# Performance work log

Measured on AMD Instinct MI355X. Metric: run time of the kernel, lower is better.

Reference implementation:

```python
import jax, jax.numpy as jnp
import numpy as np

N = 50000          # site nodes
L = 32             # max URL token length
E = 64             # embed_size
H = 128            # hidden_size
E_SIM = 800000     # edges per relation in blocks
E_SUB = 200000     # 'sim' edges classified at the end
NEG = 0.01         # LeakyReLU negative slope

def leaky(x):
    return jnp.where(x >= 0, x, NEG * x)

def lstm_final(x, mask, Wih, Whh, b, reverse):
    # x: [N, L, E], mask: [N, L] bool. Returns packed-sequence final hidden [N, E].
    if reverse:
        x = x[:, ::-1, :]
        mask = mask[:, ::-1]
    h0 = jnp.zeros((x.shape[0], Whh.shape[1]), x.dtype)
    def step(carry, inp):
        h, c = carry
        xt, mt = inp
        g = xt @ Wih.T + h @ Whh.T + b
        i, f, gg, o = jnp.split(g, 4, axis=-1)  # PyTorch gate order i,f,g,o
        cn = jax.nn.sigmoid(f) * c + jax.nn.sigmoid(i) * jnp.tanh(gg)
        hn = jax.nn.sigmoid(o) * jnp.tanh(cn)
        m = mt[:, None]
        return (jnp.where(m, hn, h), jnp.where(m, cn, c)), None
    (h, _), _ = jax.lax.scan(step, (h0, h0), (x.transpose(1, 0, 2), mask.T))
    return h

def graph_conv(h, src, dst, W, b):
    # DGL GraphConv, norm='both': D_dst^{-1/2} A D_src^{-1/2} h W + b  (degrees clamped to >=1)
    n = h.shape[0]
    ones = jnp.ones(src.shape[0], h.dtype)
    out_deg = jnp.clip(jax.ops.segment_sum(ones, src, num_segments=n), 1.0)
    in_deg = jnp.clip(jax.ops.segment_sum(ones, dst, num_segments=n), 1.0)
    feat = h * jax.lax.rsqrt(out_deg)[:, None]
    if W.shape[0] > W.shape[1]:
        feat = feat @ W  # project before gather/scatter when in_dim > out_dim (as DGL does)
        rst = jax.ops.segment_sum(feat[src], dst, num_segments=n)
    else:
        rst = jax.ops.segment_sum(feat[src], dst, num_segments=n) @ W
    return rst * jax.lax.rsqrt(in_deg)[:, None] + b

def setup_inputs():
    key = jax.random.key(0)
    ks = iter(jax.random.split(key, 64))
    def nrm(shape, scale=0.05):
        return jax.random.normal(next(ks), shape, dtype=jnp.float32) * scale
    inp = {}
    inp["inputs_s"] = jax.random.randint(next(ks), (N, L), 0, 128)
    lengths = jax.random.randint(next(ks), (N,), 1, L + 1)
    inp["inputs_sm"] = (jnp.arange(L)[None, :] < lengths[:, None]).astype(jnp.int32)
    inp["inputs_c"] = jax.random.randint(next(ks), (N, 1), 0, 101)
    inp["inputs_co"] = jax.random.randint(next(ks), (N, 1), 0, 92)
    inp["inputs_sl"] = jax.random.randint(next(ks), (N, 1), 0, 6)
    for name, m in [("sim_src", E_SIM), ("sim_dst", E_SIM), ("user_src", E_SIM),
                    ("user_dst", E_SIM), ("esub_src", E_SUB), ("esub_dst", E_SUB)]:
        inp[name] = jax.random.randint(next(ks), (m,), 0, N)
    inp["emb_url"] = nrm((128, E)); inp["emb_cat"] = nrm((101, E))
    inp["emb_country"] = nrm((92, E)); inp["emb_sl"] = nrm((6, E))
    for d in ("f", "b"):
        inp["Wih_" + d] = nrm((4 * E, E)); inp["Whh_" + d] = nrm((4 * E, E))
        inp["b_" + d] = nrm((4 * E,))  # b_ih + b_hh folded into one bias
    inp["fc_W"] = nrm((E, 2 * E)); inp["fc_b"] = nrm((E,))
    for i, din in enumerate([4 * E, H]):
        for rel in ("sim", "user"):
            inp["gcn%d_%s_W" % (i, rel)] = nrm((din, H))
            inp["gcn%d_%s_b" % (i, rel)] = nrm((H,))
    inp["cls_W1"] = nrm((H, 2 * H)); inp["cls_b1"] = nrm((H,))
    inp["bn_g"] = jnp.ones((H,), jnp.float32); inp["bn_b"] = jnp.zeros((H,), jnp.float32)
    inp["cls_W2"] = nrm((2, H)); inp["cls_b2"] = nrm((2,))
    return inp

def reference(inputs_s, inputs_sm, inputs_c, inputs_co, inputs_sl,
              sim_src, sim_dst, user_src, user_dst, esub_src, esub_dst,
              emb_url, emb_cat, emb_country, emb_sl,
              Wih_f, Whh_f, b_f, Wih_b, Whh_b, b_b, fc_W, fc_b,
              gcn0_sim_W, gcn0_sim_b, gcn0_user_W, gcn0_user_b,
              gcn1_sim_W, gcn1_sim_b, gcn1_user_W, gcn1_user_b,
              cls_W1, cls_b1, bn_g, bn_b, cls_W2, cls_b2):
    mask = inputs_sm.astype(bool)
    x = emb_url[inputs_s]                                # [N, L, E]
    hf = lstm_final(x, mask, Wih_f, Whh_f, b_f, False)   # h_n[0]
    hb = lstm_final(x, mask, Wih_b, Whh_b, b_b, True)    # h_n[1]
    h_url = leaky(jnp.concatenate([hf, hb], -1) @ fc_W.T + fc_b)  # dropout = identity (eval)
    h = jnp.concatenate([h_url, emb_cat[inputs_c[:, 0]],
                         emb_country[inputs_co[:, 0]], emb_sl[inputs_sl[:, 0]]], -1)  # [N, 4E]
    layers = [(gcn0_sim_W, gcn0_sim_b, gcn0_user_W, gcn0_user_b),
              (gcn1_sim_W, gcn1_sim_b, gcn1_user_W, gcn1_user_b)]
    for Ws, bs, Wu, bu in layers:  # HeteroGraphConv aggregate='sum'
        h = leaky(graph_conv(h, sim_src, sim_dst, Ws, bs)
                  + graph_conv(h, user_src, user_dst, Wu, bu))
    feat = jnp.concatenate([h[esub_src], h[esub_dst]], -1)  # [E_SUB, 2H]
    z = feat @ cls_W1.T + cls_b1
    z = (z - z.mean(0)) * jax.lax.rsqrt(z.var(0) + 1e-5) * bn_g + bn_b  # BatchNorm1d (batch stats)
    z = jnp.maximum(z, 0.0)
    return z @ cls_W2.T + cls_b2
```

## Files before the change

kernel.cpp:

```cpp
#include <hip/hip_runtime.h>
#include <hip/hip_bf16.h>
#include <stdint.h>

#define N_NODES 50000
#define SEQ_L   32
#define NE_BIG  800000
#define NE_SUB  200000
#define DSTRIDE 64

typedef __hip_bfloat16 bf16;
typedef unsigned short u16;
typedef _Float16 f16;
typedef _Float16 v8h __attribute__((ext_vector_type(8)));
typedef float v4f __attribute__((ext_vector_type(4)));

__device__ __forceinline__ float b2f(bf16 x) { return __bfloat162float(x); }
__device__ __forceinline__ float leakyf(float v) { return v >= 0.f ? v : 0.01f * v; }
__device__ __forceinline__ u16 f2h_bits(float x) { f16 h = (f16)x; u16 b; __builtin_memcpy(&b, &h, 2); return b; }
__device__ __forceinline__ float h2f(u16 b) { f16 h; __builtin_memcpy(&h, &b, 2); return (float)h; }
__device__ __forceinline__ uint pack2h(float a, float b) { return (uint)f2h_bits(a) | ((uint)f2h_bits(b) << 16); }

__device__ __forceinline__ float ldf(const void* p, int i, int isbf) {
  return isbf ? b2f(((const bf16*)p)[i]) : ((const float*)p)[i];
}

__device__ __forceinline__ int detect_isbf(const u16* __restrict__ u) {
  __shared__ int insane;
  if (threadIdx.x == 0) insane = 0;
  __syncthreads();
  int expo = (u[threadIdx.x * 2] >> 7) & 0xFF;
  if (expo >= 147) atomicAdd(&insane, 1);
  __syncthreads();
  return insane == 0;
}

struct PrepArgs {
  const void* Whh_f; const void* Whh_b; const void* fc_W; const void* cls_W1;
  const void* g0sW; const void* g0uW; const void* g1sW; const void* g1uW;
  const void* emb_cat; const void* emb_country; const void* emb_sl;
  const void* fc_b; const void* cls_b1; const void* g0sb; const void* g0ub;
  const void* g1sb; const void* g1ub; const void* bn_g; const void* bn_b;
  const void* cls_W2; const void* cls_b2;
  const void* emb_url; const void* Wih_f; const void* b_f; const void* Wih_b; const void* b_b;
  f16* Whh_h; u16* Bfc; u16* BW1; u16* Bg0; u16* Bg1;
  u16* embc_h; u16* embco_h; u16* embs_h;
  float* fcb; float* b1; float* g0sbP; float* g0ubP; float* g1sbP; float* g1ubP;
  float* bngP; float* bnbP; float* W2P; float* b2P;
  int* cnt4; int* cnt33; int* cur33; float* bnsums; int* dflag;
  float* Xperm;
};

__global__ __launch_bounds__(256) void prep_mega_kernel(PrepArgs A) {
  const int b = blockIdx.x;
  const int t = threadIdx.x;
  const int isbf = detect_isbf((const u16*)A.emb_url);
  auto cpy = [&](const void* s, float* d, int n, int boff) {
    int i = (b - boff) * 256 + t;
    if (i < n) d[i] = ldf(s, i, isbf);
  };
  auto cvh = [&](const void* s, u16* d, int n, int boff) {
    int i = (b - boff) * 256 + t;
    if (i < n) d[i] = f2h_bits(ldf(s, i, isbf));
  };
  auto trh = [&](const void* s, u16* d, int R, int C, int KOFF, int boff) {
    int i = (b - boff) * 256 + t;
    if (i < R * C) { int r = i / C, c = i % C; d[c * 256 + KOFF + r] = f2h_bits(ldf(s, i, isbf)); }
  };
  if      (b <   64) cvh(A.Whh_f, (u16*)A.Whh_h, 16384, 0);
  else if (b <  128) cvh(A.Whh_b, (u16*)(A.Whh_h + 16384), 16384, 64);
  else if (b <  160) cvh(A.fc_W, A.Bfc, 8192, 128);
  else if (b <  288) cvh(A.cls_W1, A.BW1, 32768, 160);
  else if (b <  416) trh(A.g0sW, A.Bg0, 256, 128, 0, 288);
  else if (b <  544) trh(A.g0uW, A.Bg0 + 128 * 256, 256, 128, 0, 416);
  else if (b <  608) trh(A.g1sW, A.Bg1, 128, 128, 0, 544);
  else if (b <  672) trh(A.g1uW, A.Bg1, 128, 128, 128, 608);
  else if (b <  698) cvh(A.emb_cat, A.embc_h, 6464, 672);
  else if (b <  721) cvh(A.emb_country, A.embco_h, 5888, 698);
  else if (b <  723) cvh(A.emb_sl, A.embs_h, 384, 721);
  else if (b <  724) cpy(A.fc_b, A.fcb, 64, 723);
  else if (b <  725) cpy(A.cls_b1, A.b1, 128, 724);
  else if (b <  726) cpy(A.g0sb, A.g0sbP, 128, 725);
  else if (b <  727) cpy(A.g0ub, A.g0ubP, 128, 726);
  else if (b <  728) cpy(A.g1sb, A.g1sbP, 128, 727);
  else if (b <  729) cpy(A.g1ub, A.g1ubP, 128, 728);
  else if (b <  730) cpy(A.bn_g, A.bngP, 128, 729);
  else if (b <  731) cpy(A.bn_b, A.bnbP, 128, 730);
  else if (b <  732) cpy(A.cls_W2, A.W2P, 256, 731);
  else if (b <  733) cpy(A.cls_b2, A.b2P, 2, 732);
  else if (b < 1515) {
    int i = (b - 733) * 256 + t;
    if (i < 4 * N_NODES) A.cnt4[i] = 0;
  } else if (b < 1516) {
    if (t < 64) { A.cnt33[t] = 0; A.cur33[t] = 0; }
    A.bnsums[t] = 0.f;
    if (t == 0) A.dflag[0] = isbf;
  } else {
    int bb = b - 1516;
    int dir = bb >> 7;
    int v = bb & 127;
    const void* Wih = dir ? A.Wih_b : A.Wih_f;
    const void* bias = dir ? A.b_b : A.b_f;
    __shared__ float embL[64];
    if (t < 64) embL[t] = ldf(A.emb_url, v * 64 + t, isbf);
    __syncthreads();
    float acc = ldf(bias, t, isbf);
#pragma unroll 8
    for (int j = 0; j < 64; ++j) acc += embL[j] * ldf(Wih, t * 64 + j, isbf);
    int g = t >> 6, unit = t & 63;
    A.Xperm[(size_t)dir * 128 * 256 + v * 256 + unit * 4 + g] = acc;
  }
}
#define PREP_BLOCKS 1772

__global__ __launch_bounds__(256) void graph_build_kernel(
    const int* __restrict__ sm, int* __restrict__ lens, int* __restrict__ cnt33,
    const int* __restrict__ s0, const int* __restrict__ d0,
    const int* __restrict__ s1, const int* __restrict__ d1,
    int* __restrict__ cnt4, int* __restrict__ col0, int* __restrict__ col1)
{
  const int b = blockIdx.x, t = threadIdx.x;
  const int NBL = (N_NODES + 255) / 256;
  const int NBE = (NE_BIG + 255) / 256;
  if (b < NBL) {
    int i = b * 256 + t;
    if (i >= N_NODES) return;
    int len = 0;
#pragma unroll
    for (int tt = 0; tt < SEQ_L; ++tt) len += sm[i * SEQ_L + tt];
    lens[i] = len;
    atomicAdd(&cnt33[len], 1);
  } else {
    int rel = (b - NBL) / NBE;
    int e = ((b - NBL) % NBE) * 256 + t;
    if (e >= NE_BIG) return;
    const int* s = rel ? s1 : s0;
    const int* d = rel ? d1 : d0;
    int* col = rel ? col1 : col0;
    int* base = cnt4 + (size_t)rel * 2 * N_NODES;
    int sv = s[e], dv = d[e];
    atomicAdd(&base[sv], 1);
    int p = atomicAdd(&base[N_NODES + dv], 1);
    if (p < DSTRIDE) col[(size_t)dv * DSTRIDE + p] = sv;
  }
}
#define GB_BLOCKS (196 + 2 * 3125)

__global__ __launch_bounds__(256) void permfill_rsq_kernel(
    const int* __restrict__ lens, const int* __restrict__ cnt33, int* __restrict__ cur33,
    int* __restrict__ perm,
    const int* __restrict__ cnt4, float* __restrict__ rsq4)
{
  const int b = blockIdx.x, t = threadIdx.x;
  const int NBL = (N_NODES + 255) / 256;
  if (b < NBL) {
    int i = b * 256 + t;
    if (i >= N_NODES) return;
    int len = lens[i];
    int base = 0;
    for (int l = len + 1; l <= SEQ_L; ++l) base += cnt33[l];
    int p = atomicAdd(&cur33[len], 1);
    perm[base + p] = i;
  } else {
    int i = (b - NBL) * 256 + t;
    if (i >= 4 * N_NODES) return;
    int c = cnt4[i]; if (c < 1) c = 1;
    rsq4[i] = __builtin_amdgcn_rsqf((float)c);
  }
}
#define PR_BLOCKS (196 + 782)

__global__ __launch_bounds__(256, 3) void lstm_mfma_kernel(
    const int* __restrict__ perm, const int* __restrict__ lens,
    const int* __restrict__ toksg,
    const float* __restrict__ Xperm,
    const f16* __restrict__ Whh_h,
    u16* __restrict__ hcat_h,
    int nnodes)
{
  __shared__ __align__(16) f16 H[2][64 * 72];
  __shared__ int toksL[2][64];
  __shared__ int permL[64];
  __shared__ int lensL[64];
  __shared__ int smax;
  const int tid = threadIdx.x;
  const int w = tid >> 6;
  const int lane = tid & 63;
  const int quad = lane >> 4;
  const int lid = lane & 15;
  const int dir = blockIdx.y;

  if (tid < 64) {
    int gid = blockIdx.x * 64 + tid;
    int node = -1, len = 0;
    if (gid < nnodes) { node = perm[gid]; len = lens[node]; }
    permL[tid] = node; lensL[tid] = len;
  }
  if (tid == 0) smax = 0;
  for (int i = tid; i < 64 * 72; i += 256) { H[0][i] = (f16)0.f; H[1][i] = (f16)0.f; }
  __syncthreads();
  if (tid < 64 && lensL[tid] > 0) atomicMax(&smax, lensL[tid]);
  __syncthreads();
  const int tmax = smax;

  const f16* Wd = Whh_h + (size_t)dir * 256 * 64;
  v8h Bf[4][2];
#pragma unroll
  for (int g = 0; g < 4; ++g)
#pragma unroll
    for (int kf = 0; kf < 2; ++kf)
      Bf[g][kf] = *(const v8h*)(Wd + (g * 64 + w * 16 + lid) * 64 + kf * 32 + quad * 8);

  int lenv[16];
#pragma unroll
  for (int mt = 0; mt < 4; ++mt)
#pragma unroll
    for (int r = 0; r < 4; ++r) lenv[mt * 4 + r] = lensL[mt * 16 + quad * 4 + r];

  float creg[16];
  f16 hreg[16];
#pragma unroll
  for (int i = 0; i < 16; ++i) { creg[i] = 0.f; hreg[i] = (f16)0.f; }

  const float* Xp = Xperm + (size_t)dir * 128 * 256;

  if (tid < 64) {
    int len = lensL[tid];
    int tok = 0;
    if (len > 0) tok = toksg[(size_t)permL[tid] * SEQ_L + (dir ? (len - 1) : 0)];
    toksL[0][tid] = tok;
  }
  __syncthreads();

  for (int step = 0; step < tmax; ++step) {
    const int rb = step & 1, wb = rb ^ 1;
#pragma unroll
    for (int mt = 0; mt < 4; ++mt) {
      float4 xr[4];
#pragma unroll
      for (int r = 0; r < 4; ++r) {
        int nd = mt * 16 + quad * 4 + r;
        xr[r] = *(const float4*)(Xp + (size_t)toksL[rb][nd] * 256 + (w * 16 + lid) * 4);
      }
      const f16* hb = &H[rb][0];
      int arow = (mt * 16 + lid) * 72 + quad * 8;
      v8h a0 = *(const v8h*)(hb + arow);
      v8h a1 = *(const v8h*)(hb + arow + 32);
      v4f acc[4];
#pragma unroll
      for (int g = 0; g < 4; ++g) {
        v4f a = {0.f, 0.f, 0.f, 0.f};
        a = __builtin_amdgcn_mfma_f32_16x16x32_f16(a0, Bf[g][0], a, 0, 0, 0);
        a = __builtin_amdgcn_mfma_f32_16x16x32_f16(a1, Bf[g][1], a, 0, 0, 0);
        acc[g] = a;
      }
#pragma unroll
      for (int r = 0; r < 4; ++r) {
        int idx = mt * 4 + r;
        int nd = mt * 16 + quad * 4 + r;
        bool act = step < lenv[idx];
        float gi = acc[0][r] + xr[r].x;
        float gf = acc[1][r] + xr[r].y;
        float gG = acc[2][r] + xr[r].z;
        float go = acc[3][r] + xr[r].w;
        float A = __expf(-gi);
        float B = __expf(-gf);
        float C = __expf(-go);
        float D = __expf(2.f * fminf(gG, 15.f));
        float sf = __builtin_amdgcn_rcpf(1.f + B);
        float sitg = (D - 1.f) * __builtin_amdgcn_rcpf((1.f + A) * (D + 1.f));
        float cn = sf * creg[idx] + sitg;
        float E = __expf(2.f * fminf(cn, 15.f));
        float hn = (E - 1.f) * __builtin_amdgcn_rcpf((1.f + C) * (E + 1.f));
        if (act) { creg[idx] = cn; hreg[idx] = (f16)hn; }
        H[wb][nd * 72 + w * 16 + lid] = hreg[idx];
      }
    }
    if (tid < 64 && step + 1 < tmax) {
      int len = lensL[tid];
      int tok = 0;
      if (step + 1 < len) {
        int t = dir ? (len - 2 - step) : (step + 1);
        tok = toksg[(size_t)permL[tid] * SEQ_L + t];
      }
      toksL[wb][tid] = tok;
    }
    __syncthreads();
  }
#pragma unroll
  for (int mt = 0; mt < 4; ++mt)
#pragma unroll
    for (int r = 0; r < 4; ++r) {
      int nd = mt * 16 + quad * 4 + r;
      int gnode = permL[nd];
      if (gnode >= 0) {
        u16 bits; f16 hv = hreg[mt * 4 + r]; __builtin_memcpy(&bits, &hv, 2);
        hcat_h[(size_t)gnode * 128 + dir * 64 + w * 16 + lid] = bits;
      }
    }
}

template<int K, int COLS, int AMODE, bool LEAKY, int OHS, bool EMB, bool BNS>
__global__ __launch_bounds__(256) void mfma_gemm(
    const u16* __restrict__ Ah,
    const int* __restrict__ esrc, const int* __restrict__ edst, const u16* __restrict__ Fh,
    const u16* __restrict__ B,
    const float* __restrict__ bias, const float* __restrict__ bias2,
    const float* __restrict__ rs0, const float* __restrict__ rs1,
    u16* __restrict__ outh0, u16* __restrict__ outh1,
    const int* __restrict__ ic, const int* __restrict__ ico, const int* __restrict__ isl,
    const u16* __restrict__ ech, const u16* __restrict__ ecoh, const u16* __restrict__ eslh,
    float* __restrict__ bnsums,
    int nrows)
{
  constexpr int AST = K + 8;
  constexpr int ABYTES = 64 * AST * 2;
  constexpr int EBYTES = 64 * 129 * 4;
  constexpr int SBYTES = (ABYTES > EBYTES) ? ABYTES : EBYTES;
  __shared__ __align__(16) char smem[SBYTES];
  u16* As = (u16*)smem;
  float* Es = (float*)smem;
  __shared__ int idxL[128];
  __shared__ float bnred[BNS ? 512 : 1];

  const int tid = threadIdx.x;
  const int w = tid >> 6;
  const int lane = tid & 63;
  const int quad = lane >> 4;
  const int lid = lane & 15;
  const int r0 = blockIdx.x * 64;

  if (AMODE == 2) {
    if (tid < 64) {
      int row = r0 + tid;
      idxL[tid] = (row < nrows) ? esrc[row] : -1;
      idxL[64 + tid] = (row < nrows) ? edst[row] : -1;
    }
    __syncthreads();
    for (int idx = tid; idx < 64 * (K / 8); idx += 256) {
      int rn = idx / (K / 8), seg = idx % (K / 8);
      int half = seg >> 4, k8 = seg & 15;
      int base = idxL[half * 64 + rn];
      uint4 v = {0u, 0u, 0u, 0u};
      if (base >= 0) v = *(const uint4*)(Fh + (size_t)base * 128 + k8 * 8);
      *(uint4*)(As + rn * AST + seg * 8) = v;
    }
  } else {
    for (int idx = tid; idx < 64 * (K / 8); idx += 256) {
      int rn = idx / (K / 8), c8 = idx % (K / 8);
      int row = r0 + rn;
      uint4 v = {0u, 0u, 0u, 0u};
      if (row < nrows) v = *(const uint4*)(Ah + (size_t)row * K + c8 * 8);
      *(uint4*)(As + rn * AST + c8 * 8) = v;
    }
  }
  __syncthreads();

  constexpr int NT = COLS / 16;
  v4f acc[NT];
#pragma unroll
  for (int i = 0; i < NT; ++i) acc[i] = (v4f){0.f, 0.f, 0.f, 0.f};

  for (int kb = 0; kb < K / 32; ++kb) {
    v8h a = *(const v8h*)((const f16*)As + (w * 16 + lid) * AST + kb * 32 + quad * 8);
#pragma unroll
    for (int ct = 0; ct < NT; ++ct) {
      v8h b = *(const v8h*)((const f16*)B + (size_t)(ct * 16 + lid) * K + kb * 32 + quad * 8);
      acc[ct] = __builtin_amdgcn_mfma_f32_16x16x32_f16(a, b, acc[ct], 0, 0, 0);
    }
  }

  constexpr int NH = (COLS > 128) ? 2 : 1;
  constexpr int CH = COLS / NH;
  float bs = 0.f, bs2 = 0.f;
#pragma unroll
  for (int h = 0; h < NH; ++h) {
    __syncthreads();
#pragma unroll
    for (int ct = 0; ct < CH / 16; ++ct) {
      int ctg = h * (CH / 16) + ct;
#pragma unroll
      for (int r = 0; r < 4; ++r)
        Es[(w * 16 + quad * 4 + r) * 129 + ct * 16 + lid] = acc[ctg][r];
    }
    __syncthreads();
    for (int idx = tid; idx < 64 * CH; idx += 256) {
      int rn = idx / CH, c = idx % CH;
      int row = r0 + rn;
      float v = 0.f;
      if (row < nrows) {
        v = Es[rn * 129 + c];
        if (bias) v += bias[h * CH + c];
        if (bias2) v += bias2[h * CH + c];
        if (LEAKY) v = leakyf(v);
        const float* rs = (h == 0) ? rs0 : rs1;
        if (rs) v *= rs[row];
        u16* oh = (h == 0) ? outh0 : outh1;
        oh[(size_t)row * OHS + c] = f2h_bits(v);
      }
      if (BNS) { bs += v; bs2 += v * v; }
    }
  }
  if (BNS) {
    bnred[tid] = bs;
    bnred[256 + tid] = bs2;
    __syncthreads();
    if (tid < 128) {
      atomicAdd(&bnsums[tid], bnred[tid] + bnred[tid + 128]);
      atomicAdd(&bnsums[128 + tid], bnred[256 + tid] + bnred[384 + tid]);
    }
  }
  if (EMB) {
    for (int idx = tid; idx < 64 * 192; idx += 256) {
      int rn = idx / 192, j = idx % 192;
      int row = r0 + rn;
      if (row >= nrows) continue;
      u16 v;
      if (j < 64)       v = ech [ic [row] * 64 + j];
      else if (j < 128) v = ecoh[ico[row] * 64 + (j - 64)];
      else              v = eslh[isl[row] * 64 + (j - 128)];
      outh0[(size_t)row * OHS + 64 + j] = v;
    }
  }
}

__global__ __launch_bounds__(256) void gather_merge0_kernel(
    const int* __restrict__ colS, const int* __restrict__ cntS, const u16* __restrict__ Ps,
    const int* __restrict__ colU, const int* __restrict__ cntU, const u16* __restrict__ Pu,
    const float* __restrict__ rsS, const float* __restrict__ rsU,
    const float* __restrict__ bS, const float* __restrict__ bU,
    u16* __restrict__ outh, int nnodes)
{
  int wave = threadIdx.x >> 6;
  int lane = threadIdx.x & 63;
  int node = __builtin_amdgcn_readfirstlane(blockIdx.x * 4 + wave);
  if (node >= nnodes) return;
  const uint* PS2 = (const uint*)Ps;
  const uint* PU2 = (const uint*)Pu;
  float2 aS = make_float2(0.f, 0.f), aU = make_float2(0.f, 0.f);
  {
    const int* col = colS + (size_t)node * DSTRIDE;
    int cnt = min(cntS[node], DSTRIDE);
    int e = 0;
    for (; e + 4 <= cnt; e += 4) {
      uint v0 = PS2[(size_t)col[e] * 64 + lane];
      uint v1 = PS2[(size_t)col[e + 1] * 64 + lane];
      uint v2 = PS2[(size_t)col[e + 2] * 64 + lane];
      uint v3 = PS2[(size_t)col[e + 3] * 64 + lane];
      aS.x += h2f((u16)v0) + h2f((u16)v1) + h2f((u16)v2) + h2f((u16)v3);
      aS.y += h2f((u16)(v0 >> 16)) + h2f((u16)(v1 >> 16)) + h2f((u16)(v2 >> 16)) + h2f((u16)(v3 >> 16));
    }
    for (; e < cnt; ++e) {
      uint v = PS2[(size_t)col[e] * 64 + lane];
      aS.x += h2f((u16)v); aS.y += h2f((u16)(v >> 16));
    }
  }
  {
    const int* col = colU + (size_t)node * DSTRIDE;
    int cnt = min(cntU[node], DSTRIDE);
    int e = 0;
    for (; e + 4 <= cnt; e += 4) {
      uint v0 = PU2[(size_t)col[e] * 64 + lane];
      uint v1 = PU2[(size_t)col[e + 1] * 64 + lane];
      uint v2 = PU2[(size_t)col[e + 2] * 64 + lane];
      uint v3 = PU2[(size_t)col[e + 3] * 64 + lane];
      aU.x += h2f((u16)v0) + h2f((u16)v1) + h2f((u16)v2) + h2f((u16)v3);
      aU.y += h2f((u16)(v0 >> 16)) + h2f((u16)(v1 >> 16)) + h2f((u16)(v2 >> 16)) + h2f((u16)(v3 >> 16));
    }
    for (; e < cnt; ++e) {
      uint v = PU2[(size_t)col[e] * 64 + lane];
      aU.x += h2f((u16)v); aU.y += h2f((u16)(v >> 16));
    }
  }
  float rS = rsS[node], rU = rsU[node];
  float2 bsv = ((const float2*)bS)[lane];
  float2 buv = ((const float2*)bU)[lane];
  float o0 = leakyf(aS.x * rS + bsv.x + aU.x * rU + buv.x);
  float o1 = leakyf(aS.y * rS + bsv.y + aU.y * rU + buv.y);
  ((uint*)outh)[(size_t)node * 64 + lane] = pack2h(o0, o1);
}

__global__ __launch_bounds__(256) void gather_cat1_kernel(
    const int* __restrict__ colS, const int* __restrict__ cntS,
    const int* __restrict__ colU, const int* __restrict__ cntU,
    const u16* __restrict__ Fh,
    const float* __restrict__ rsoutS, const float* __restrict__ rsoutU,
    const float* __restrict__ rsinS, const float* __restrict__ rsinU,
    u16* __restrict__ Acat, int nnodes)
{
  int wave = threadIdx.x >> 6;
  int lane = threadIdx.x & 63;
  int node = __builtin_amdgcn_readfirstlane(blockIdx.x * 4 + wave);
  if (node >= nnodes) return;
  const uint* F2 = (const uint*)Fh;
  float2 aS = make_float2(0.f, 0.f), aU = make_float2(0.f, 0.f);
  {
    const int* col = colS + (size_t)node * DSTRIDE;
    int cnt = min(cntS[node], DSTRIDE);
    int e = 0;
    for (; e + 2 <= cnt; e += 2) {
      int s0 = col[e], s1 = col[e + 1];
      float c0 = rsoutS[s0], c1 = rsoutS[s1];
      uint v0 = F2[(size_t)s0 * 64 + lane];
      uint v1 = F2[(size_t)s1 * 64 + lane];
      aS.x += c0 * h2f((u16)v0) + c1 * h2f((u16)v1);
      aS.y += c0 * h2f((u16)(v0 >> 16)) + c1 * h2f((u16)(v1 >> 16));
    }
    for (; e < cnt; ++e) {
      int s = col[e]; float c = rsoutS[s];
      uint v = F2[(size_t)s * 64 + lane];
      aS.x += c * h2f((u16)v); aS.y += c * h2f((u16)(v >> 16));
    }
  }
  {
    const int* col = colU + (size_t)node * DSTRIDE;
    int cnt = min(cntU[node], DSTRIDE);
    int e = 0;
    for (; e + 2 <= cnt; e += 2) {
      int s0 = col[e], s1 = col[e + 1];
      float c0 = rsoutU[s0], c1 = rsoutU[s1];
      uint v0 = F2[(size_t)s0 * 64 + lane];
      uint v1 = F2[(size_t)s1 * 64 + lane];
      aU.x += c0 * h2f((u16)v0) + c1 * h2f((u16)v1);
      aU.y += c0 * h2f((u16)(v0 >> 16)) + c1 * h2f((u16)(v1 >> 16));
    }
    for (; e < cnt; ++e) {
      int s = col[e]; float c = rsoutU[s];
      uint v = F2[(size_t)s * 64 + lane];
      aU.x += c * h2f((u16)v); aU.y += c * h2f((u16)(v >> 16));
    }
  }
  float rs = rsinS[node], ru = rsinU[node];
  ((uint*)Acat)[(size_t)node * 128 + lane] = pack2h(aS.x * rs, aS.y * rs);
  ((uint*)Acat)[(size_t)node * 128 + 64 + lane] = pack2h(aU.x * ru, aU.y * ru);
}

__global__ __launch_bounds__(256) void out_kernel(
    const u16* __restrict__ zh, const float* __restrict__ bnsums,
    const float* __restrict__ g, const float* __restrict__ bb, float M,
    const float* __restrict__ W2, const float* __restrict__ b2,
    void* __restrict__ out, int Mi, const int* __restrict__ flag)
{
  __shared__ float lds[128 * 65];
  __shared__ float red[64 * 8];
  __shared__ float ssL[256];
  const int tid = threadIdx.x;
  const int n = tid & 63;
  const int q = __builtin_amdgcn_readfirstlane(tid >> 6);
  const int r0 = blockIdx.x * 64;
  if (tid < 128) {
    float mean = bnsums[tid] / M;
    float var = bnsums[128 + tid] / M - mean * mean;
    float sc = g[tid] * __builtin_amdgcn_rsqf(var + 1e-5f);
    ssL[tid] = sc;
    ssL[128 + tid] = bb[tid] - mean * sc;
  }
  for (int idx = tid; idx < 64 * 128; idx += 256) {
    int rn = idx >> 7, j = idx & 127;
    int row = r0 + rn;
    lds[j * 65 + rn] = (row < Mi) ? h2f(zh[(size_t)row * 128 + j]) : 0.f;
  }
  __syncthreads();
  float a0 = 0.f, a1 = 0.f;
#pragma unroll 8
  for (int jj = 0; jj < 32; ++jj) {
    int j = q * 32 + jj;
    float y = lds[j * 65 + n] * ssL[j] + ssL[128 + j];
    y = y > 0.f ? y : 0.f;
    a0 += y * W2[j];
    a1 += y * W2[128 + j];
  }
  red[n * 8 + q * 2 + 0] = a0;
  red[n * 8 + q * 2 + 1] = a1;
  __syncthreads();
  if (q == 0 && (r0 + n) < Mi) {
    float o0 = red[n * 8] + red[n * 8 + 2] + red[n * 8 + 4] + red[n * 8 + 6] + b2[0];
    float o1 = red[n * 8 + 1] + red[n * 8 + 3] + red[n * 8 + 5] + red[n * 8 + 7] + b2[1];
    size_t oi = (size_t)(r0 + n) * 2;
    if (*flag) {
      ((bf16*)out)[oi + 0] = __float2bfloat16(o0);
      ((bf16*)out)[oi + 1] = __float2bfloat16(o1);
    } else {
      ((float*)out)[oi + 0] = o0;
      ((float*)out)[oi + 1] = o1;
    }
  }
}

extern "C" void kernel_launch(void* const* d_in, const int* in_sizes, int n_in,
                              void* d_out, int out_size, void* d_ws, size_t ws_size,
                              hipStream_t stream) {
  (void)in_sizes; (void)n_in; (void)out_size; (void)ws_size;
  const int N = N_NODES;
  const int* inputs_s  = (const int*)d_in[0];
  const int* inputs_sm = (const int*)d_in[1];
  const int* inputs_c  = (const int*)d_in[2];
  const int* inputs_co = (const int*)d_in[3];
  const int* inputs_sl = (const int*)d_in[4];
  const int* sim_src   = (const int*)d_in[5];
  const int* sim_dst   = (const int*)d_in[6];
  const int* user_src  = (const int*)d_in[7];
  const int* user_dst  = (const int*)d_in[8];
  const int* esub_src  = (const int*)d_in[9];
  const int* esub_dst  = (const int*)d_in[10];

  char* base = (char*)d_ws;
  size_t off = 0;
  auto alloc = [&](size_t bytes) -> char* {
    char* p = base + off;
    off += (bytes + 255) & ~(size_t)255;
    return p;
  };
  int* dflag    = (int*)alloc(256);
  f16* Whh_h    = (f16*)alloc(2 * 256 * 64 * 2);
  float* Xperm  = (float*)alloc(2 * 128 * 256 * 4);
  u16* Bfc      = (u16*)alloc(64 * 128 * 2);
  u16* BW1      = (u16*)alloc(128 * 256 * 2);
  u16* Bg0      = (u16*)alloc(256 * 256 * 2);
  u16* Bg1      = (u16*)alloc(128 * 256 * 2);
  u16* P_embc_h = (u16*)alloc(6464 * 2);
  u16* P_embco_h= (u16*)alloc(5888 * 2);
  u16* P_embs_h = (u16*)alloc(384 * 2);
  float* P_fcb  = (float*)alloc(64 * 4);
  float* P_b1   = (float*)alloc(128 * 4);
  float* P_g0sb = (float*)alloc(128 * 4);
  float* P_g0ub = (float*)alloc(128 * 4);
  float* P_g1sb = (float*)alloc(128 * 4);
  float* P_g1ub = (float*)alloc(128 * 4);
  float* P_bng  = (float*)alloc(128 * 4);
  float* P_bnb  = (float*)alloc(128 * 4);
  float* P_W2   = (float*)alloc(256 * 4);
  float* P_b2   = (float*)alloc(2 * 4);
  int* lens     = (int*)alloc((size_t)N * 4);
  int* cnt33    = (int*)alloc(64 * 4);
  int* cur33    = (int*)alloc(64 * 4);
  int* perm     = (int*)alloc((size_t)N * 4);
  int* cnt4     = (int*)alloc((size_t)4 * N * 4);
  float* rsq4   = (float*)alloc((size_t)4 * N * 4);
  float* bnsums = (float*)alloc(256 * 4);
  char* bufA = alloc((size_t)N * 256 * 4);
  char* bufB = alloc((size_t)N * 256 * 2);
  char* bufC = alloc((size_t)N * 256 * 2);
  char* bufE = alloc((size_t)N * 128 * 2);
  u16* h_h    = (u16*)bufA;
  u16* zh     = (u16*)bufA;
  int* col_sim = (int*)(bufA + (size_t)N * 256 * 2);
  int* col_usr = (int*)(bufA + (size_t)N * 256 * 2 + (size_t)N * DSTRIDE * 4);
  u16* hcat_h = (u16*)bufB;
  u16* h1_h   = (u16*)bufB;
  u16* Ps_h   = (u16*)bufC;
  u16* Pu_h   = Ps_h + (size_t)N * 128;
  u16* Acat   = (u16*)bufC;
  u16* F_h    = (u16*)bufE;

  const int NB64 = (N + 63) / 64;
  const int NBZ  = (NE_SUB + 63) / 64;

  PrepArgs PA;
  PA.Whh_f = d_in[16]; PA.Whh_b = d_in[19]; PA.fc_W = d_in[21]; PA.cls_W1 = d_in[31];
  PA.g0sW = d_in[23]; PA.g0uW = d_in[25]; PA.g1sW = d_in[27]; PA.g1uW = d_in[29];
  PA.emb_cat = d_in[12]; PA.emb_country = d_in[13]; PA.emb_sl = d_in[14];
  PA.fc_b = d_in[22]; PA.cls_b1 = d_in[32]; PA.g0sb = d_in[24]; PA.g0ub = d_in[26];
  PA.g1sb = d_in[28]; PA.g1ub = d_in[30]; PA.bn_g = d_in[33]; PA.bn_b = d_in[34];
  PA.cls_W2 = d_in[35]; PA.cls_b2 = d_in[36];
  PA.emb_url = d_in[11]; PA.Wih_f = d_in[15]; PA.b_f = d_in[17]; PA.Wih_b = d_in[18]; PA.b_b = d_in[20];
  PA.Whh_h = Whh_h; PA.Bfc = Bfc; PA.BW1 = BW1; PA.Bg0 = Bg0; PA.Bg1 = Bg1;
  PA.embc_h = P_embc_h; PA.embco_h = P_embco_h; PA.embs_h = P_embs_h;
  PA.fcb = P_fcb; PA.b1 = P_b1; PA.g0sbP = P_g0sb; PA.g0ubP = P_g0ub; PA.g1sbP = P_g1sb; PA.g1ubP = P_g1ub;
  PA.bngP = P_bng; PA.bnbP = P_bnb; PA.W2P = P_W2; PA.b2P = P_b2;
  PA.cnt4 = cnt4; PA.cnt33 = cnt33; PA.cur33 = cur33; PA.bnsums = bnsums; PA.dflag = dflag;
  PA.Xperm = Xperm;
  prep_mega_kernel<<<PREP_BLOCKS, 256, 0, stream>>>(PA);

  graph_build_kernel<<<GB_BLOCKS, 256, 0, stream>>>(inputs_sm, lens, cnt33,
                                                    sim_src, sim_dst, user_src, user_dst,
                                                    cnt4, col_sim, col_usr);

  permfill_rsq_kernel<<<PR_BLOCKS, 256, 0, stream>>>(lens, cnt33, cur33, perm, cnt4, rsq4);

  lstm_mfma_kernel<<<dim3(NB64, 2), 256, 0, stream>>>(perm, lens, inputs_s, Xperm, Whh_h, hcat_h, N);

  mfma_gemm<128, 64, 1, true, 256, true, false><<<NB64, 256, 0, stream>>>(
      hcat_h, nullptr, nullptr, nullptr, Bfc, P_fcb, nullptr, nullptr, nullptr,
      h_h, nullptr, inputs_c, inputs_co, inputs_sl, P_embc_h, P_embco_h, P_embs_h, nullptr, N);

  mfma_gemm<256, 256, 1, false, 128, false, false><<<NB64, 256, 0, stream>>>(
      h_h, nullptr, nullptr, nullptr, Bg0, nullptr, nullptr, rsq4, rsq4 + 2 * N,
      Ps_h, Pu_h, nullptr, nullptr, nullptr, nullptr, nullptr, nullptr, nullptr, N);

  gather_merge0_kernel<<<(N + 3) / 4, 256, 0, stream>>>(col_sim, cnt4 + N, Ps_h,
                                                        col_usr, cnt4 + 3 * N, Pu_h,
                                                        rsq4 + N, rsq4 + 3 * N, P_g0sb, P_g0ub, h1_h, N);

  gather_cat1_kernel<<<(N + 3) / 4, 256, 0, stream>>>(col_sim, cnt4 + N, col_usr, cnt4 + 3 * N, h1_h,
                                                      rsq4, rsq4 + 2 * N, rsq4 + N, rsq4 + 3 * N, Acat, N);

  mfma_gemm<256, 128, 1, true, 128, false, false><<<NB64, 256, 0, stream>>>(
      Acat, nullptr, nullptr, nullptr, Bg1, P_g1sb, P_g1ub, nullptr, nullptr,
      F_h, nullptr, nullptr, nullptr, nullptr, nullptr, nullptr, nullptr, nullptr, N);

  mfma_gemm<256, 128, 2, false, 128, false, true><<<NBZ, 256, 0, stream>>>(
      nullptr, esub_src, esub_dst, F_h, BW1, P_b1, nullptr, nullptr, nullptr,
      zh, nullptr, nullptr, nullptr, nullptr, nullptr, nullptr, nullptr, bnsums, NE_SUB);

  out_kernel<<<NBZ, 256, 0, stream>>>(zh, bnsums, P_bng, P_bnb, (float)NE_SUB,
                                      P_W2, P_b2, d_out, NE_SUB, dflag);
}
```

Baseline: 1.163 ms.

## Fuse fc+embedding with layer-0 projection and gather with layer-1 GEMM

The fc GEMM, embedding concatenation and the layer-0 GCN projection now run in one kernel, so the 256-wide node features stay in shared memory instead of round-tripping through global memory. The layer-1 neighbour gather is fused with its MFMA GEMM, which removes the Acat intermediate buffer. The graph-build kernel processes four edges per thread with int4 loads. A trade-off is that the fused gather runs one 64-node block per 256 threads, with each wave gathering 16 nodes serially, so there is less parallelism for latency hiding in the irregular gather.

```diff
diff --git a/kernel.cpp b/kernel.cpp
--- a/kernel.cpp
+++ b/kernel.cpp
@@ -120,7 +120,7 @@
 {
   const int b = blockIdx.x, t = threadIdx.x;
   const int NBL = (N_NODES + 255) / 256;
-  const int NBE = (NE_BIG + 255) / 256;
+  const int NBE4 = (NE_BIG + 1023) / 1024;
   if (b < NBL) {
     int i = b * 256 + t;
     if (i >= N_NODES) return;
@@ -130,20 +130,39 @@
     lens[i] = len;
     atomicAdd(&cnt33[len], 1);
   } else {
-    int rel = (b - NBL) / NBE;
-    int e = ((b - NBL) % NBE) * 256 + t;
-    if (e >= NE_BIG) return;
+    int rel = (b - NBL) / NBE4;
+    int e4 = (((b - NBL) % NBE4) * 256 + t) * 4;
+    if (e4 >= NE_BIG) return;
     const int* s = rel ? s1 : s0;
     const int* d = rel ? d1 : d0;
     int* col = rel ? col1 : col0;
     int* base = cnt4 + (size_t)rel * 2 * N_NODES;
-    int sv = s[e], dv = d[e];
-    atomicAdd(&base[sv], 1);
-    int p = atomicAdd(&base[N_NODES + dv], 1);
-    if (p < DSTRIDE) col[(size_t)dv * DSTRIDE + p] = sv;
-  }
-}
-#define GB_BLOCKS (196 + 2 * 3125)
+    if (e4 + 4 <= NE_BIG) {
+      int4 sv = *(const int4*)(s + e4);
+      int4 dv = *(const int4*)(d + e4);
+      atomicAdd(&base[sv.x], 1);
+      atomicAdd(&base[sv.y], 1);
+      atomicAdd(&base[sv.z], 1);
+      atomicAdd(&base[sv.w], 1);
+      int p0 = atomicAdd(&base[N_NODES + dv.x], 1);
+      int p1 = atomicAdd(&base[N_NODES + dv.y], 1);
+      int p2 = atomicAdd(&base[N_NODES + dv.z], 1);
+      int p3 = atomicAdd(&base[N_NODES + dv.w], 1);
+      if (p0 < DSTRIDE) col[(size_t)dv.x * DSTRIDE + p0] = sv.x;
+      if (p1 < DSTRIDE) col[(size_t)dv.y * DSTRIDE + p1] = sv.y;
+      if (p2 < DSTRIDE) col[(size_t)dv.z * DSTRIDE + p2] = sv.z;
+      if (p3 < DSTRIDE) col[(size_t)dv.w * DSTRIDE + p3] = sv.w;
+    } else {
+      for (int e = e4; e < NE_BIG; ++e) {
+        int sv = s[e], dv = d[e];
+        atomicAdd(&base[sv], 1);
+        int p = atomicAdd(&base[N_NODES + dv], 1);
+        if (p < DSTRIDE) col[(size_t)dv * DSTRIDE + p] = sv;
+      }
+    }
+  }
+}
+#define GB_BLOCKS (196 + 2 * 782)
 
 __global__ __launch_bounds__(256) void permfill_rsq_kernel(
     const int* __restrict__ lens, const int* __restrict__ cnt33, int* __restrict__ cur33,
@@ -299,126 +318,96 @@
     }
 }
 
-template<int K, int COLS, int AMODE, bool LEAKY, int OHS, bool EMB, bool BNS>
-__global__ __launch_bounds__(256) void mfma_gemm(
-    const u16* __restrict__ Ah,
-    const int* __restrict__ esrc, const int* __restrict__ edst, const u16* __restrict__ Fh,
-    const u16* __restrict__ B,
-    const float* __restrict__ bias, const float* __restrict__ bias2,
-    const float* __restrict__ rs0, const float* __restrict__ rs1,
-    u16* __restrict__ outh0, u16* __restrict__ outh1,
+__global__ __launch_bounds__(256) void fc_emb_proj_kernel(
+    const u16* __restrict__ hcat,
+    const u16* __restrict__ Bfc,
+    const float* __restrict__ fcb,
     const int* __restrict__ ic, const int* __restrict__ ico, const int* __restrict__ isl,
     const u16* __restrict__ ech, const u16* __restrict__ ecoh, const u16* __restrict__ eslh,
-    float* __restrict__ bnsums,
+    const u16* __restrict__ Bg0,
+    const float* __restrict__ rsOutS, const float* __restrict__ rsOutU,
+    u16* __restrict__ Ps, u16* __restrict__ Pu,
     int nrows)
 {
-  constexpr int AST = K + 8;
-  constexpr int ABYTES = 64 * AST * 2;
-  constexpr int EBYTES = 64 * 129 * 4;
-  constexpr int SBYTES = (ABYTES > EBYTES) ? ABYTES : EBYTES;
-  __shared__ __align__(16) char smem[SBYTES];
-  u16* As = (u16*)smem;
+  __shared__ __align__(16) char smem[33792 + 17408];
+  u16* As2 = (u16*)smem;
+  u16* As1 = (u16*)(smem + 33792);
   float* Es = (float*)smem;
-  __shared__ int idxL[128];
-  __shared__ float bnred[BNS ? 512 : 1];
-
   const int tid = threadIdx.x;
-  const int w = tid >> 6;
-  const int lane = tid & 63;
-  const int quad = lane >> 4;
-  const int lid = lane & 15;
+  const int w = tid >> 6, lane = tid & 63, quad = lane >> 4, lid = lane & 15;
   const int r0 = blockIdx.x * 64;
 
-  if (AMODE == 2) {
-    if (tid < 64) {
-      int row = r0 + tid;
-      idxL[tid] = (row < nrows) ? esrc[row] : -1;
-      idxL[64 + tid] = (row < nrows) ? edst[row] : -1;
-    }
-    __syncthreads();
-    for (int idx = tid; idx < 64 * (K / 8); idx += 256) {
-      int rn = idx / (K / 8), seg = idx % (K / 8);
-      int half = seg >> 4, k8 = seg & 15;
-      int base = idxL[half * 64 + rn];
-      uint4 v = {0u, 0u, 0u, 0u};
-      if (base >= 0) v = *(const uint4*)(Fh + (size_t)base * 128 + k8 * 8);
-      *(uint4*)(As + rn * AST + seg * 8) = v;
-    }
-  } else {
-    for (int idx = tid; idx < 64 * (K / 8); idx += 256) {
-      int rn = idx / (K / 8), c8 = idx % (K / 8);
-      int row = r0 + rn;
-      uint4 v = {0u, 0u, 0u, 0u};
-      if (row < nrows) v = *(const uint4*)(Ah + (size_t)row * K + c8 * 8);
-      *(uint4*)(As + rn * AST + c8 * 8) = v;
-    }
-  }
-  __syncthreads();
-
-  constexpr int NT = COLS / 16;
-  v4f acc[NT];
-#pragma unroll
-  for (int i = 0; i < NT; ++i) acc[i] = (v4f){0.f, 0.f, 0.f, 0.f};
-
-  for (int kb = 0; kb < K / 32; ++kb) {
-    v8h a = *(const v8h*)((const f16*)As + (w * 16 + lid) * AST + kb * 32 + quad * 8);
-#pragma unroll
-    for (int ct = 0; ct < NT; ++ct) {
-      v8h b = *(const v8h*)((const f16*)B + (size_t)(ct * 16 + lid) * K + kb * 32 + quad * 8);
-      acc[ct] = __builtin_amdgcn_mfma_f32_16x16x32_f16(a, b, acc[ct], 0, 0, 0);
-    }
-  }
-
-  constexpr int NH = (COLS > 128) ? 2 : 1;
-  constexpr int CH = COLS / NH;
-  float bs = 0.f, bs2 = 0.f;
-#pragma unroll
-  for (int h = 0; h < NH; ++h) {
-    __syncthreads();
-#pragma unroll
-    for (int ct = 0; ct < CH / 16; ++ct) {
-      int ctg = h * (CH / 16) + ct;
-#pragma unroll
-      for (int r = 0; r < 4; ++r)
-        Es[(w * 16 + quad * 4 + r) * 129 + ct * 16 + lid] = acc[ctg][r];
-    }
-    __syncthreads();
-    for (int idx = tid; idx < 64 * CH; idx += 256) {
-      int rn = idx / CH, c = idx % CH;
-      int row = r0 + rn;
-      float v = 0.f;
-      if (row < nrows) {
-        v = Es[rn * 129 + c];
-        if (bias) v += bias[h * CH + c];
-        if (bias2) v += bias2[h * CH + c];
-        if (LEAKY) v = leakyf(v);
-        const float* rs = (h == 0) ? rs0 : rs1;
-        if (rs) v *= rs[row];
-        u16* oh = (h == 0) ? outh0 : outh1;
-        oh[(size_t)row * OHS + c] = f2h_bits(v);
-      }
-      if (BNS) { bs += v; bs2 += v * v; }
-    }
-  }
-  if (BNS) {
-    bnred[tid] = bs;
-    bnred[256 + tid] = bs2;
-    __syncthreads();
-    if (tid < 128) {
-      atomicAdd(&bnsums[tid], bnred[tid] + bnred[tid + 128]);
-      atomicAdd(&bnsums[128 + tid], bnred[256 + tid] + bnred[384 + tid]);
-    }
-  }
-  if (EMB) {
-    for (int idx = tid; idx < 64 * 192; idx += 256) {
-      int rn = idx / 192, j = idx % 192;
-      int row = r0 + rn;
-      if (row >= nrows) continue;
-      u16 v;
+  for (int idx = tid; idx < 64 * 16; idx += 256) {
+    int rn = idx >> 4, c8 = idx & 15;
+    int row = r0 + rn;
+    uint4 v = {0u, 0u, 0u, 0u};
+    if (row < nrows) v = *(const uint4*)(hcat + (size_t)row * 128 + c8 * 8);
+    *(uint4*)(As1 + rn * 136 + c8 * 8) = v;
+  }
+  for (int idx = tid; idx < 64 * 192; idx += 256) {
+    int rn = idx / 192, j = idx % 192;
+    int row = r0 + rn;
+    u16 v = 0;
+    if (row < nrows) {
       if (j < 64)       v = ech [ic [row] * 64 + j];
       else if (j < 128) v = ecoh[ico[row] * 64 + (j - 64)];
       else              v = eslh[isl[row] * 64 + (j - 128)];
-      outh0[(size_t)row * OHS + 64 + j] = v;
+    }
+    As2[rn * 264 + 64 + j] = v;
+  }
+  __syncthreads();
+
+  v4f acc1[4];
+#pragma unroll
+  for (int i = 0; i < 4; ++i) acc1[i] = (v4f){0.f, 0.f, 0.f, 0.f};
+  for (int kb = 0; kb < 4; ++kb) {
+    v8h a = *(const v8h*)((const f16*)As1 + (w * 16 + lid) * 136 + kb * 32 + quad * 8);
+#pragma unroll
+    for (int ct = 0; ct < 4; ++ct) {
+      v8h bfr = *(const v8h*)((const f16*)Bfc + (size_t)(ct * 16 + lid) * 128 + kb * 32 + quad * 8);
+      acc1[ct] = __builtin_amdgcn_mfma_f32_16x16x32_f16(a, bfr, acc1[ct], 0, 0, 0);
+    }
+  }
+#pragma unroll
+  for (int ct = 0; ct < 4; ++ct)
+#pragma unroll
+    for (int r = 0; r < 4; ++r) {
+      float v = acc1[ct][r] + fcb[ct * 16 + lid];
+      As2[(w * 16 + quad * 4 + r) * 264 + ct * 16 + lid] = f2h_bits(leakyf(v));
+    }
+  __syncthreads();
+
+  v4f acc2[16];
+#pragma unroll
+  for (int i = 0; i < 16; ++i) acc2[i] = (v4f){0.f, 0.f, 0.f, 0.f};
+  for (int kb = 0; kb < 8; ++kb) {
+    v8h a = *(const v8h*)((const f16*)As2 + (w * 16 + lid) * 264 + kb * 32 + quad * 8);
+#pragma unroll
+    for (int ct = 0; ct < 16; ++ct) {
+      v8h bfr = *(const v8h*)((const f16*)Bg0 + (size_t)(ct * 16 + lid) * 256 + kb * 32 + quad * 8);
+      acc2[ct] = __builtin_amdgcn_mfma_f32_16x16x32_f16(a, bfr, acc2[ct], 0, 0, 0);
+    }
+  }
+#pragma unroll
+  for (int h = 0; h < 2; ++h) {
+    __syncthreads();
+#pragma unroll
+    for (int ct = 0; ct < 8; ++ct) {
+      int ctg = h * 8 + ct;
+#pragma unroll
+      for (int r = 0; r < 4; ++r)
+        Es[(w * 16 + quad * 4 + r) * 129 + ct * 16 + lid] = acc2[ctg][r];
+    }
+    __syncthreads();
+    for (int idx = tid; idx < 64 * 128; idx += 256) {
+      int rn = idx >> 7, c = idx & 127;
+      int row = r0 + rn;
+      if (row >= nrows) continue;
+      float v = Es[rn * 129 + c];
+      const float* rs = (h == 0) ? rsOutS : rsOutU;
+      v *= rs[row];
+      u16* oh = (h == 0) ? Ps : Pu;
+      oh[(size_t)row * 128 + c] = f2h_bits(v);
     }
   }
 }
@@ -479,59 +468,168 @@
   ((uint*)outh)[(size_t)node * 64 + lane] = pack2h(o0, o1);
 }
 
-__global__ __launch_bounds__(256) void gather_cat1_kernel(
+__global__ __launch_bounds__(256) void gather_g1_kernel(
     const int* __restrict__ colS, const int* __restrict__ cntS,
     const int* __restrict__ colU, const int* __restrict__ cntU,
     const u16* __restrict__ Fh,
     const float* __restrict__ rsoutS, const float* __restrict__ rsoutU,
     const float* __restrict__ rsinS, const float* __restrict__ rsinU,
-    u16* __restrict__ Acat, int nnodes)
+    const u16* __restrict__ Bg1,
+    const float* __restrict__ g1sb, const float* __restrict__ g1ub,
+    u16* __restrict__ outF, int nnodes)
 {
-  int wave = threadIdx.x >> 6;
-  int lane = threadIdx.x & 63;
-  int node = __builtin_amdgcn_readfirstlane(blockIdx.x * 4 + wave);
-  if (node >= nnodes) return;
+  __shared__ __align__(16) char smem[33792];
+  u16* As2 = (u16*)smem;
+  uint* As2u = (uint*)smem;
+  float* Es = (float*)smem;
+  const int tid = threadIdx.x;
+  const int w = tid >> 6, lane = tid & 63, quad = lane >> 4, lid = lane & 15;
+  const int r0 = blockIdx.x * 64;
   const uint* F2 = (const uint*)Fh;
-  float2 aS = make_float2(0.f, 0.f), aU = make_float2(0.f, 0.f);
-  {
-    const int* col = colS + (size_t)node * DSTRIDE;
-    int cnt = min(cntS[node], DSTRIDE);
-    int e = 0;
-    for (; e + 2 <= cnt; e += 2) {
-      int s0 = col[e], s1 = col[e + 1];
-      float c0 = rsoutS[s0], c1 = rsoutS[s1];
-      uint v0 = F2[(size_t)s0 * 64 + lane];
-      uint v1 = F2[(size_t)s1 * 64 + lane];
-      aS.x += c0 * h2f((u16)v0) + c1 * h2f((u16)v1);
-      aS.y += c0 * h2f((u16)(v0 >> 16)) + c1 * h2f((u16)(v1 >> 16));
-    }
-    for (; e < cnt; ++e) {
-      int s = col[e]; float c = rsoutS[s];
-      uint v = F2[(size_t)s * 64 + lane];
-      aS.x += c * h2f((u16)v); aS.y += c * h2f((u16)(v >> 16));
-    }
-  }
-  {
-    const int* col = colU + (size_t)node * DSTRIDE;
-    int cnt = min(cntU[node], DSTRIDE);
-    int e = 0;
-    for (; e + 2 <= cnt; e += 2) {
-      int s0 = col[e], s1 = col[e + 1];
-      float c0 = rsoutU[s0], c1 = rsoutU[s1];
-      uint v0 = F2[(size_t)s0 * 64 + lane];
-      uint v1 = F2[(size_t)s1 * 64 + lane];
-      aU.x += c0 * h2f((u16)v0) + c1 * h2f((u16)v1);
-      aU.y += c0 * h2f((u16)(v0 >> 16)) + c1 * h2f((u16)(v1 >> 16));
-    }
-    for (; e < cnt; ++e) {
-      int s = col[e]; float c = rsoutU[s];
-      uint v = F2[(size_t)s * 64 + lane];
-      aU.x += c * h2f((u16)v); aU.y += c * h2f((u16)(v >> 16));
-    }
-  }
-  float rs = rsinS[node], ru = rsinU[node];
-  ((uint*)Acat)[(size_t)node * 128 + lane] = pack2h(aS.x * rs, aS.y * rs);
-  ((uint*)Acat)[(size_t)node * 128 + 64 + lane] = pack2h(aU.x * ru, aU.y * ru);
+
+  for (int i = 0; i < 16; ++i) {
+    int nl = w * 16 + i;
+    int node = r0 + nl;
+    float2 aS = make_float2(0.f, 0.f), aU = make_float2(0.f, 0.f);
+    float rs = 0.f, ru = 0.f;
+    if (node < nnodes) {
+      {
+        const int* col = colS + (size_t)node * DSTRIDE;
+        int cnt = min(cntS[node], DSTRIDE);
+        int e = 0;
+        for (; e + 2 <= cnt; e += 2) {
+          int s0 = col[e], s1 = col[e + 1];
+          float c0 = rsoutS[s0], c1 = rsoutS[s1];
+          uint v0 = F2[(size_t)s0 * 64 + lane];
+          uint v1 = F2[(size_t)s1 * 64 + lane];
+          aS.x += c0 * h2f((u16)v0) + c1 * h2f((u16)v1);
+          aS.y += c0 * h2f((u16)(v0 >> 16)) + c1 * h2f((u16)(v1 >> 16));
+        }
+        for (; e < cnt; ++e) {
+          int s = col[e]; float c = rsoutS[s];
+          uint v = F2[(size_t)s * 64 + lane];
+          aS.x += c * h2f((u16)v); aS.y += c * h2f((u16)(v >> 16));
+        }
+      }
+      {
+        const int* col = colU + (size_t)node * DSTRIDE;
+        int cnt = min(cntU[node], DSTRIDE);
+        int e = 0;
+        for (; e + 2 <= cnt; e += 2) {
+          int s0 = col[e], s1 = col[e + 1];
+          float c0 = rsoutU[s0], c1 = rsoutU[s1];
+          uint v0 = F2[(size_t)s0 * 64 + lane];
+          uint v1 = F2[(size_t)s1 * 64 + lane];
+          aU.x += c0 * h2f((u16)v0) + c1 * h2f((u16)v1);
+          aU.y += c0 * h2f((u16)(v0 >> 16)) + c1 * h2f((u16)(v1 >> 16));
+        }
+        for (; e < cnt; ++e) {
+          int s = col[e]; float c = rsoutU[s];
+          uint v = F2[(size_t)s * 64 + lane];
+          aU.x += c * h2f((u16)v); aU.y += c * h2f((u16)(v >> 16));
+        }
+      }
+      rs = rsinS[node]; ru = rsinU[node];
+    }
+    As2u[nl * 132 + lane] = pack2h(aS.x * rs, aS.y * rs);
+    As2u[nl * 132 + 64 + lane] = pack2h(aU.x * ru, aU.y * ru);
+  }
+  __syncthreads();
+
+  v4f acc[8];
+#pragma unroll
+  for (int i = 0; i < 8; ++i) acc[i] = (v4f){0.f, 0.f, 0.f, 0.f};
+  for (int kb = 0; kb < 8; ++kb) {
+    v8h a = *(const v8h*)((const f16*)As2 + (w * 16 + lid) * 264 + kb * 32 + quad * 8);
+#pragma unroll
+    for (int ct = 0; ct < 8; ++ct) {
+      v8h bfr = *(const v8h*)((const f16*)Bg1 + (size_t)(ct * 16 + lid) * 256 + kb * 32 + quad * 8);
+      acc[ct] = __builtin_amdgcn_mfma_f32_16x16x32_f16(a, bfr, acc[ct], 0, 0, 0);
+    }
+  }
+  __syncthreads();
+#pragma unroll
+  for (int ct = 0; ct < 8; ++ct)
+#pragma unroll
+    for (int r = 0; r < 4; ++r)
+      Es[(w * 16 + quad * 4 + r) * 129 + ct * 16 + lid] = acc[ct][r];
+  __syncthreads();
+  for (int idx = tid; idx < 64 * 128; idx += 256) {
+    int rn = idx >> 7, c = idx & 127;
+    int row = r0 + rn;
+    if (row >= nnodes) continue;
+    float v = Es[rn * 129 + c] + g1sb[c] + g1ub[c];
+    outF[(size_t)row * 128 + c] = f2h_bits(leakyf(v));
+  }
+}
+
+__global__ __launch_bounds__(256) void zgemm_kernel(
+    const int* __restrict__ esrc, const int* __restrict__ edst, const u16* __restrict__ Fh,
+    const u16* __restrict__ B,
+    const float* __restrict__ bias,
+    u16* __restrict__ outh, float* __restrict__ bnsums, int nrows)
+{
+  __shared__ __align__(16) char smem[34048];
+  u16* As = (u16*)smem;
+  float* Es = (float*)smem;
+  __shared__ int idxL[128];
+  __shared__ float bnred[512];
+  const int tid = threadIdx.x;
+  const int w = tid >> 6, lane = tid & 63, quad = lane >> 4, lid = lane & 15;
+  const int r0 = blockIdx.x * 64;
+
+  if (tid < 64) {
+    int row = r0 + tid;
+    idxL[tid] = (row < nrows) ? esrc[row] : -1;
+    idxL[64 + tid] = (row < nrows) ? edst[row] : -1;
+  }
+  __syncthreads();
+  for (int idx = tid; idx < 64 * 32; idx += 256) {
+    int rn = idx >> 5, seg = idx & 31;
+    int half = seg >> 4, k8 = seg & 15;
+    int base = idxL[half * 64 + rn];
+    uint4 v = {0u, 0u, 0u, 0u};
+    if (base >= 0) v = *(const uint4*)(Fh + (size_t)base * 128 + k8 * 8);
+    *(uint4*)(As + rn * 264 + seg * 8) = v;
+  }
+  __syncthreads();
+
+  v4f acc[8];
+#pragma unroll
+  for (int i = 0; i < 8; ++i) acc[i] = (v4f){0.f, 0.f, 0.f, 0.f};
+  for (int kb = 0; kb < 8; ++kb) {
+    v8h a = *(const v8h*)((const f16*)As + (w * 16 + lid) * 264 + kb * 32 + quad * 8);
+#pragma unroll
+    for (int ct = 0; ct < 8; ++ct) {
+      v8h bfr = *(const v8h*)((const f16*)B + (size_t)(ct * 16 + lid) * 256 + kb * 32 + quad * 8);
+      acc[ct] = __builtin_amdgcn_mfma_f32_16x16x32_f16(a, bfr, acc[ct], 0, 0, 0);
+    }
+  }
+  __syncthreads();
+#pragma unroll
+  for (int ct = 0; ct < 8; ++ct)
+#pragma unroll
+    for (int r = 0; r < 4; ++r)
+      Es[(w * 16 + quad * 4 + r) * 129 + ct * 16 + lid] = acc[ct][r];
+  __syncthreads();
+  float bs = 0.f, bs2 = 0.f;
+  for (int idx = tid; idx < 64 * 128; idx += 256) {
+    int rn = idx >> 7, c = idx & 127;
+    int row = r0 + rn;
+    float v = 0.f;
+    if (row < nrows) {
+      v = Es[rn * 129 + c] + bias[c];
+      outh[(size_t)row * 128 + c] = f2h_bits(v);
+    }
+    bs += v; bs2 += v * v;
+  }
+  bnred[tid] = bs;
+  bnred[256 + tid] = bs2;
+  __syncthreads();
+  if (tid < 128) {
+    atomicAdd(&bnsums[tid], bnred[tid] + bnred[tid + 128]);
+    atomicAdd(&bnsums[128 + tid], bnred[256 + tid] + bnred[384 + tid]);
+  }
 }
 
 __global__ __launch_bounds__(256) void out_kernel(
@@ -641,15 +739,13 @@
   char* bufB = alloc((size_t)N * 256 * 2);
   char* bufC = alloc((size_t)N * 256 * 2);
   char* bufE = alloc((size_t)N * 128 * 2);
-  u16* h_h    = (u16*)bufA;
-  u16* zh     = (u16*)bufA;
+  u16* zh      = (u16*)bufA;
   int* col_sim = (int*)(bufA + (size_t)N * 256 * 2);
   int* col_usr = (int*)(bufA + (size_t)N * 256 * 2 + (size_t)N * DSTRIDE * 4);
   u16* hcat_h = (u16*)bufB;
   u16* h1_h   = (u16*)bufB;
   u16* Ps_h   = (u16*)bufC;
   u16* Pu_h   = Ps_h + (size_t)N * 128;
-  u16* Acat   = (u16*)bufC;
   u16* F_h    = (u16*)bufE;
 
   const int NB64 = (N + 63) / 64;
@@ -679,28 +775,20 @@
 
   lstm_mfma_kernel<<<dim3(NB64, 2), 256, 0, stream>>>(perm, lens, inputs_s, Xperm, Whh_h, hcat_h, N);
 
-  mfma_gemm<128, 64, 1, true, 256, true, false><<<NB64, 256, 0, stream>>>(
-      hcat_h, nullptr, nullptr, nullptr, Bfc, P_fcb, nullptr, nullptr, nullptr,
-      h_h, nullptr, inputs_c, inputs_co, inputs_sl, P_embc_h, P_embco_h, P_embs_h, nullptr, N);
-
-  mfma_gemm<256, 256, 1, false, 128, false, false><<<NB64, 256, 0, stream>>>(
-      h_h, nullptr, nullptr, nullptr, Bg0, nullptr, nullptr, rsq4, rsq4 + 2 * N,
-      Ps_h, Pu_h, nullptr, nullptr, nullptr, nullptr, nullptr, nullptr, nullptr, N);
+  fc_emb_proj_kernel<<<NB64, 256, 0, stream>>>(hcat_h, Bfc, P_fcb,
+                                               inputs_c, inputs_co, inputs_sl,
+                                               P_embc_h, P_embco_h, P_embs_h,
+                                               Bg0, rsq4, rsq4 + 2 * N, Ps_h, Pu_h, N);
 
   gather_merge0_kernel<<<(N + 3) / 4, 256, 0, stream>>>(col_sim, cnt4 + N, Ps_h,
                                                         col_usr, cnt4 + 3 * N, Pu_h,
                                                         rsq4 + N, rsq4 + 3 * N, P_g0sb, P_g0ub, h1_h, N);
 
-  gather_cat1_kernel<<<(N + 3) / 4, 256, 0, stream>>>(col_sim, cnt4 + N, col_usr, cnt4 + 3 * N, h1_h,
-                                                      rsq4, rsq4 + 2 * N, rsq4 + N, rsq4 + 3 * N, Acat, N);
-
-  mfma_gemm<256, 128, 1, true, 128, false, false><<<NB64, 256, 0, stream>>>(
-      Acat, nullptr, nullptr, nullptr, Bg1, P_g1sb, P_g1ub, nullptr, nullptr,
-      F_h, nullptr, nullptr, nullptr, nullptr, nullptr, nullptr, nullptr, nullptr, N);
-
-  mfma_gemm<256, 128, 2, false, 128, false, true><<<NBZ, 256, 0, stream>>>(
-      nullptr, esub_src, esub_dst, F_h, BW1, P_b1, nullptr, nullptr, nullptr,
-      zh, nullptr, nullptr, nullptr, nullptr, nullptr, nullptr, nullptr, bnsums, NE_SUB);
+  gather_g1_kernel<<<NB64, 256, 0, stream>>>(col_sim, cnt4 + N, col_usr, cnt4 + 3 * N, h1_h,
+                                             rsq4, rsq4 + 2 * N, rsq4 + N, rsq4 + 3 * N,
+                                             Bg1, P_g1sb, P_g1ub, F_h, N);
+
+  zgemm_kernel<<<NBZ, 256, 0, stream>>>(esub_src, esub_dst, F_h, BW1, P_b1, zh, bnsums, NE_SUB);
 
   out_kernel<<<NBZ, 256, 0, stream>>>(zh, bnsums, P_bng, P_bnb, (float)NE_SUB,
                                       P_W2, P_b2, d_out, NE_SUB, dflag);
```

Result: slower. 1.270 ms (+9.2%).
